# Optimization experiments

Measured on AMD Instinct MI355X. Metric: run time of the kernel, lower is better.

Reference implementation:

```python
import jax, jax.numpy as jnp
import numpy as np


def setup_inputs() -> dict:
    key = jax.random.key(0)
    ks = jax.random.split(key, 12)
    N, F, S = 50000, 256, 20          # node_num, feature_dim, samp_num
    B = 8192                          # batch of target nodes
    L1, L2 = 256, 128                 # layer1_dim, layer2_dim
    D1, D2 = 256, 256                 # dec1_dim, dec2_dim
    inv = lambda d: 1.0 / np.sqrt(d)
    return {
        "features": jax.random.normal(ks[0], (N, F), jnp.float32),
        "neigh1": jax.random.randint(ks[1], (N, S), 0, N),   # sampled neighbors (layer 1)
        "neigh2": jax.random.randint(ks[2], (B, S), 0, N),   # sampled neighbors of batch nodes
        "eps": jax.random.normal(ks[3], (B, L2), jnp.float32),
        "W1": jax.random.normal(ks[4], (L1, F), jnp.float32) * inv(F),
        "W2": jax.random.normal(ks[5], (L2, L1), jnp.float32) * inv(L1),
        "W3": jax.random.normal(ks[6], (L2, L1), jnp.float32) * inv(L1),
        "Wd1": jax.random.normal(ks[7], (D1, L2), jnp.float32) * inv(L2),
        "b1": jnp.zeros((D1,), jnp.float32),
        "Wd2": jax.random.normal(ks[8], (D2, D1), jnp.float32) * inv(D1),
        "b2": jnp.zeros((D2,), jnp.float32),
        "M1": jax.random.normal(ks[9], (D2, D2), jnp.float32) * inv(D2),
        "M2": jax.random.normal(ks[10], (D2, D2), jnp.float32) * inv(D2),
    }


def reference(features, neigh1, neigh2, eps, W1, W2, W3, Wd1, b1, Wd2, b2, M1, M2):
    # --- encode: GraphSAGE mean-aggregate, gcn=True encoder (no self-concat) ---
    # layer 1: aggregate raw features over sampled neighbors for every node
    agg1 = jnp.mean(features[neigh1], axis=1)            # [N, F]
    h1 = jax.nn.relu(agg1 @ W1.T)                        # [N, L1]
    # layer 2: aggregate layer-1 embeddings over the batch nodes' sampled neighbors
    agg2 = jnp.mean(h1[neigh2], axis=1)                  # [B, L1]
    mu = jax.nn.relu(agg2 @ W2.T)                        # [B, L2]  (enc2)
    logvar = jax.nn.relu(agg2 @ W3.T)                    # [B, L2]  (enc3)
    # --- reparameterize: std = exp(logvar), h = eps*std + mu ---
    h = eps * jnp.exp(logvar) + mu                       # [B, L2]
    # --- decode ---
    o = jnp.tanh(h @ Wd1.T + b1)                         # [B, D1]
    o = o @ Wd2.T + b2                                   # [B, D2]
    emb1 = o @ M1                                        # [B, D2]
    emb2 = o @ M2                                        # [B, D2]
    # --- inner product decoder (logits, no sigmoid) ---
    adj_without_sigmoid = emb1 @ emb2.T                  # [B, B]
    return (mu, logvar, adj_without_sigmoid)
```

## Files before the change

### kernel.cpp

```cpp
#include <hip/hip_runtime.h>
#include <cstdint>
#include <cstddef>

typedef unsigned short u16;
typedef unsigned int   u32;
typedef unsigned char  u8;
typedef __attribute__((ext_vector_type(8))) short short8;
typedef __attribute__((ext_vector_type(8))) u16   u16x8;
typedef __attribute__((ext_vector_type(4))) float f32x4;
typedef __attribute__((ext_vector_type(2))) float f32x2;
typedef __attribute__((ext_vector_type(4))) u16   u16x4;

__device__ __forceinline__ float bf2f(u16 u){
  u32 x = ((u32)u) << 16; float f; __builtin_memcpy(&f, &x, 4); return f;
}
__device__ __forceinline__ u16 f2bf(float f){
  u32 x; __builtin_memcpy(&x, &f, 4);
  x += 0x7fffu + ((x >> 16) & 1u);
  return (u16)(x >> 16);
}

__device__ __forceinline__ void gload_lds16(const u16* g, u16* l){
  __builtin_amdgcn_global_load_lds((const __attribute__((address_space(1))) void*)g,
                                   (__attribute__((address_space(3))) void*)l, 16, 0, 0);
}

__global__ __launch_bounds__(256)
void prep(const float* __restrict__ M2v, const float* __restrict__ M1v,
          const float* __restrict__ W1, const float* __restrict__ W2,
          const float* __restrict__ W3, const float* __restrict__ Wd1,
          const float* __restrict__ Wd2,
          u16* __restrict__ Gtb, u16* __restrict__ W1b, u16* __restrict__ Wcb,
          u16* __restrict__ Wd1b, u16* __restrict__ Wd2b)
{
  __shared__ u16 lds[32768];
  const int tid = threadIdx.x;
  if (blockIdx.x >= 4){
    int j = (blockIdx.x - 4) * 256 + tid;
    const float* src; u16* dst;
    if (j < 16384)                { src = W1;  dst = W1b; }
    else if ((j -= 16384) < 8192) { src = W2;  dst = Wcb; }
    else if ((j -= 8192)  < 8192) { src = W3;  dst = Wcb + 32768; }
    else if ((j -= 8192)  < 8192) { src = Wd1; dst = Wd1b; }
    else { j -= 8192; src = Wd2; dst = Wd2b; }
    float4 v = ((const float4*)src)[j];
    u16x4 o; o[0]=f2bf(v.x); o[1]=f2bf(v.y); o[2]=f2bf(v.z); o[3]=f2bf(v.w);
    ((u16x4*)dst)[j] = o;
    return;
  }
  u16* As0 = lds;         u16* As1 = lds + 8192;
  u16* Bs0 = lds + 16384; u16* Bs1 = lds + 24576;
  const int lane = tid & 63;
  const int wave = tid >> 6;
  const int wm = wave >> 1, wn = wave & 1;
  const int m0 = (blockIdx.x >> 1) << 7, n0 = (blockIdx.x & 1) << 7;

  f32x4 acc[4][4];
  #pragma unroll
  for (int a = 0; a < 4; ++a)
    #pragma unroll
    for (int b = 0; b < 4; ++b)
      acc[a][b] = (f32x4){0.f, 0.f, 0.f, 0.f};

  auto stage = [&](int buf, int kt){
    const int k0 = kt * 64;
    u16* Ad = buf ? As1 : As0;
    u16* Bd = buf ? Bs1 : Bs0;
    const int f = tid * 32;
    {
      const float* sA = M2v + (size_t)(m0 + (f >> 6)) * 256 + k0 + (f & 63);
      u16 t[32];
      #pragma unroll
      for (int q = 0; q < 8; ++q){
        float4 v = *(const float4*)(sA + q * 4);
        t[q*4]=f2bf(v.x); t[q*4+1]=f2bf(v.y); t[q*4+2]=f2bf(v.z); t[q*4+3]=f2bf(v.w);
      }
      #pragma unroll
      for (int q = 0; q < 4; ++q)
        *(u16x8*)(&Ad[f + q*8]) = *(const u16x8*)(&t[q*8]);
    }
    {
      const float* sB = M1v + (size_t)(n0 + (f >> 6)) * 256 + k0 + (f & 63);
      u16 t[32];
      #pragma unroll
      for (int q = 0; q < 8; ++q){
        float4 v = *(const float4*)(sB + q * 4);
        t[q*4]=f2bf(v.x); t[q*4+1]=f2bf(v.y); t[q*4+2]=f2bf(v.z); t[q*4+3]=f2bf(v.w);
      }
      #pragma unroll
      for (int q = 0; q < 4; ++q)
        *(u16x8*)(&Bd[f + q*8]) = *(const u16x8*)(&t[q*8]);
    }
  };

  stage(0, 0);
  __syncthreads();
  int cur = 0;
  for (int kt = 0; kt < 4; ++kt){
    if (kt < 3) stage(cur ^ 1, kt + 1);
    const u16* as = cur ? As1 : As0;
    const u16* bs = cur ? Bs1 : Bs0;
    #pragma unroll
    for (int kk = 0; kk < 2; ++kk){
      const int ko = kk * 32 + (lane >> 4) * 8;
      short8 af[4], bq[4];
      #pragma unroll
      for (int mi = 0; mi < 4; ++mi)
        af[mi] = *(const short8*)(as + (wm*64 + mi*16 + (lane & 15)) * 64 + ko);
      #pragma unroll
      for (int ni = 0; ni < 4; ++ni)
        bq[ni] = *(const short8*)(bs + (wn*64 + ni*16 + (lane & 15)) * 64 + ko);
      #pragma unroll
      for (int mi = 0; mi < 4; ++mi)
        #pragma unroll
        for (int ni = 0; ni < 4; ++ni)
          acc[mi][ni] = __builtin_amdgcn_mfma_f32_16x16x32_bf16(af[mi], bq[ni], acc[mi][ni], 0, 0, 0);
    }
    __syncthreads();
    cur ^= 1;
  }

  const int rbase = m0 + wm * 64 + ((lane >> 4) << 2);
  const int cbase = n0 + wn * 64 + (lane & 15);
  #pragma unroll
  for (int mi = 0; mi < 4; ++mi)
    #pragma unroll
    for (int ni = 0; ni < 4; ++ni){
      const int col = cbase + ni * 16;
      #pragma unroll
      for (int r = 0; r < 4; ++r)
        Gtb[(size_t)(rbase + mi * 16 + r) * 256 + col] = f2bf(acc[mi][ni][r]);
    }
}

__global__ void gather_fp8(const u32* __restrict__ rows, const int* __restrict__ idx,
                           u32* __restrict__ out, int nout){
  const int pair = blockIdx.x * 4 + (threadIdx.x >> 6);
  const int lane = threadIdx.x & 63;
  const int node0 = pair * 2;
  if (node0 >= nout) return;
  const int half = lane >> 5, l31 = lane & 31;
  const int node = node0 + half;
  const int jv = (l31 < 20) ? idx[(size_t)node * 20 + l31] : 0;
  float a[8];
  #pragma unroll
  for (int k = 0; k < 8; ++k) a[k] = 0.f;
  #pragma unroll
  for (int s = 0; s < 20; ++s){
    const int j = __shfl(jv, (lane & 32) + s, 64);
    const uint2 u = *(const uint2*)(rows + (size_t)j * 64 + l31 * 2);
    f32x2 p0 = __builtin_amdgcn_cvt_pk_f32_fp8((int)u.x, false);
    f32x2 p1 = __builtin_amdgcn_cvt_pk_f32_fp8((int)u.x, true);
    f32x2 p2 = __builtin_amdgcn_cvt_pk_f32_fp8((int)u.y, false);
    f32x2 p3 = __builtin_amdgcn_cvt_pk_f32_fp8((int)u.y, true);
    a[0]+=p0[0]; a[1]+=p0[1]; a[2]+=p1[0]; a[3]+=p1[1];
    a[4]+=p2[0]; a[5]+=p2[1]; a[6]+=p3[0]; a[7]+=p3[1];
  }
  const float inv = 0.05f;
  #pragma unroll
  for (int k = 0; k < 8; ++k) a[k] = fmaxf(a[k] * inv, 0.f);
  const int w0 = __builtin_amdgcn_cvt_pk_fp8_f32(a[0], a[1], 0, false);
  const int w1 = __builtin_amdgcn_cvt_pk_fp8_f32(a[2], a[3], 0, false);
  const int w2 = __builtin_amdgcn_cvt_pk_fp8_f32(a[4], a[5], 0, false);
  const int w3 = __builtin_amdgcn_cvt_pk_fp8_f32(a[6], a[7], 0, false);
  uint2 o;
  o.x = (w0 & 0xffffu) | ((u32)(w1 & 0xffffu) << 16);
  o.y = (w2 & 0xffffu) | ((u32)(w3 & 0xffffu) << 16);
  *(uint2*)(out + (size_t)node * 64 + l31 * 2) = o;
}

__global__ __launch_bounds__(512)
void adj_gemm(const u16* __restrict__ A, const u16* __restrict__ B,
              float* __restrict__ C)
{
  __shared__ __align__(16) u16 lds[32768];
  u16* As = lds;
  u16* Bs = lds + 16384;
  const int tid  = threadIdx.x;
  const int lane = tid & 63;
  const int wave = tid >> 6;
  const int wm = wave >> 2, wn = wave & 3;
  const int bid  = blockIdx.x;
  const int xcd  = bid & 7, slot = bid >> 3;
  const int m0 = ((xcd << 2) + (slot >> 5)) << 8;
  const int n0 = (slot & 31) << 8;

  f32x4 acc[8][4];
  #pragma unroll
  for (int a = 0; a < 8; ++a)
    #pragma unroll
    for (int b = 0; b < 4; ++b)
      acc[a][b] = (f32x4){0.f, 0.f, 0.f, 0.f};

  for (int kt = 0; kt < 4; ++kt){
    const int k0 = kt * 64;
    #pragma unroll
    for (int c = 0; c < 4; ++c){
      const int f = c * 4096 + tid * 8;
      const int row = f >> 6, ksw = (f & 63) ^ ((row & 7) << 3);
      gload_lds16(A + (size_t)(m0 + row) * 256 + k0 + ksw, As + f);
    }
    #pragma unroll
    for (int c = 0; c < 4; ++c){
      const int f = c * 4096 + tid * 8;
      const int row = f >> 6, ksw = (f & 63) ^ ((row & 7) << 3);
      gload_lds16(B + (size_t)(n0 + row) * 256 + k0 + ksw, Bs + f);
    }
    __syncthreads();
    #pragma unroll
    for (int kk = 0; kk < 2; ++kk){
      const int ko = kk * 32 + (lane >> 4) * 8;
      short8 af[8], bq[4];
      #pragma unroll
      for (int mi = 0; mi < 8; ++mi){
        const int row = wm*128 + mi*16 + (lane & 15);
        af[mi] = *(const short8*)(As + row * 64 + (ko ^ ((row & 7) << 3)));
      }
      #pragma unroll
      for (int ni = 0; ni < 4; ++ni){
        const int row = wn*64 + ni*16 + (lane & 15);
        bq[ni] = *(const short8*)(Bs + row * 64 + (ko ^ ((row & 7) << 3)));
      }
      #pragma unroll
      for (int mi = 0; mi < 8; ++mi)
        #pragma unroll
        for (int ni = 0; ni < 4; ++ni)
          acc[mi][ni] = __builtin_amdgcn_mfma_f32_16x16x32_bf16(af[mi], bq[ni], acc[mi][ni], 0, 0, 0);
    }
    __syncthreads();
  }

  float* T = (float*)lds;
  #pragma unroll
  for (int c = 0; c < 8; ++c){
    if (wm == (c >> 2)){
      #pragma unroll
      for (int mi2 = 0; mi2 < 2; ++mi2){
        const int mi = (c & 3) * 2 + mi2;
        #pragma unroll
        for (int ni = 0; ni < 4; ++ni){
          const int cl = wn*64 + ni*16 + (lane & 15);
          #pragma unroll
          for (int r = 0; r < 4; ++r){
            const int lr = mi2*16 + ((lane >> 4) << 2) + r;
            T[lr * 260 + cl] = acc[mi][ni][r];
          }
        }
      }
    }
    __syncthreads();
    #pragma unroll
    for (int q = 0; q < 4; ++q){
      const int g = q * 512 + tid;
      const int r = g >> 6, col = (g & 63) * 4;
      f32x4 v = *(const f32x4*)(T + r * 260 + col);
      __builtin_nontemporal_store(v, (f32x4*)(C + (size_t)(m0 + c*32 + r) * 8192 + n0 + col));
    }
    __syncthreads();
  }
}

__global__ __launch_bounds__(256)
void fw_gemm(const float* __restrict__ A, const u16* __restrict__ B,
             u8* __restrict__ C, int M)
{
  __shared__ u16 lds[26624];
  u16* As0 = lds;         u16* As1 = lds + 5120;
  u16* Bs0 = lds + 10240; u16* Bs1 = lds + 18432;
  const int tid  = threadIdx.x;
  const int lane = tid & 63;
  const int wave = tid >> 6;
  const int wm = wave >> 1, wn = wave & 1;
  const int m0 = blockIdx.x << 7;

  f32x4 acc[4][8];
  #pragma unroll
  for (int a = 0; a < 4; ++a)
    #pragma unroll
    for (int b = 0; b < 8; ++b)
      acc[a][b] = (f32x4){0.f, 0.f, 0.f, 0.f};

  auto stage = [&](int buf, int kt){
    const int k0 = kt * 32;
    u16* Ad = buf ? As1 : As0;
    u16* Bd = buf ? Bs1 : Bs0;
    const int f = tid * 16;
    const int row = f >> 5, ku = f & 31;
    int ra = m0 + row; if (ra >= M) ra = M - 1;
    const float* sA = A + (size_t)ra * 256 + k0 + ku;
    u16 t[16];
    #pragma unroll
    for (int q = 0; q < 4; ++q){
      float4 v = *(const float4*)(sA + q * 4);
      t[q*4]=f2bf(v.x); t[q*4+1]=f2bf(v.y); t[q*4+2]=f2bf(v.z); t[q*4+3]=f2bf(v.w);
    }
    u16* dA = Ad + row * 40 + ku;
    *(u16x8*)(dA)     = *(const u16x8*)(&t[0]);
    *(u16x8*)(dA + 8) = *(const u16x8*)(&t[8]);
    #pragma unroll
    for (int c = 0; c < 4; ++c){
      const int g = c * 2048 + tid * 8;
      const int rb = g >> 5, kb = g & 31;
      gload_lds16(B + (size_t)rb * 256 + k0 + (kb ^ ((rb & 3) << 3)),
                  Bd + c * 2048 + wave * 512);
    }
  };

  stage(0, 0);
  __syncthreads();
  int cur = 0;
  for (int kt = 0; kt < 8; ++kt){
    if (kt + 1 < 8) stage(cur ^ 1, kt + 1);
    const u16* as = cur ? As1 : As0;
    const u16* bs = cur ? Bs1 : Bs0;
    const int ko = (lane >> 4) * 8;
    short8 af[4], bq[8];
    #pragma unroll
    for (int mi = 0; mi < 4; ++mi)
      af[mi] = *(const short8*)(as + (wm*64 + mi*16 + (lane & 15)) * 40 + ko);
    #pragma unroll
    for (int ni = 0; ni < 8; ++ni){
      const int row = wn*128 + ni*16 + (lane & 15);
      bq[ni] = *(const short8*)(bs + row * 32 + (ko ^ ((row & 3) << 3)));
    }
    #pragma unroll
    for (int mi = 0; mi < 4; ++mi)
      #pragma unroll
      for (int ni = 0; ni < 8; ++ni)
        acc[mi][ni] = __builtin_amdgcn_mfma_f32_16x16x32_bf16(af[mi], bq[ni], acc[mi][ni], 0, 0, 0);
    __syncthreads();
    cur ^= 1;
  }

  const int rbase = m0 + wm * 64 + ((lane >> 4) << 2);
  const int cbase = wn * 128 + (lane & 15);
  #pragma unroll
  for (int mi = 0; mi < 4; ++mi)
    #pragma unroll
    for (int ni = 0; ni < 8; ++ni){
      const int col = cbase + ni * 16;
      #pragma unroll
      for (int r = 0; r < 4; ++r){
        const int row = rbase + mi * 16 + r;
        if (row < M){
          const float v = acc[mi][ni][r];
          const int pk = __builtin_amdgcn_cvt_pk_fp8_f32(v, v, 0, false);
          C[(size_t)row * 256 + col] = (u8)(pk & 0xff);
        }
      }
    }
}

__global__ __launch_bounds__(256)
void decoder(const u32* __restrict__ h1, const int* __restrict__ neigh2,
             const u16* __restrict__ Wcb,
             const u16* __restrict__ Wd1b, const u16* __restrict__ Wd2b,
             const u16* __restrict__ Gtb, const float* __restrict__ eps,
             const float* __restrict__ b1, const float* __restrict__ b2,
             float* __restrict__ outMu, float* __restrict__ outLv,
             u16* __restrict__ o2g, u16* __restrict__ tmpg)
{
  __shared__ u16 lds[38912];
  u16* S0 = lds;
  u16* S1 = lds + 16384;
  u16* H  = lds + 32768;
  u16* O1 = lds + 34816;
  const int tid = threadIdx.x;
  const int lane = tid & 63, wave = tid >> 6;
  const int m0 = blockIdx.x << 4;

  auto stageB = [&](const u16* G, int K, int k0, u16* dst){
    const int fb = wave * 4096 + lane * 8;
    #pragma unroll
    for (int c = 0; c < 8; ++c){
      int f = fb + c * 512;
      gload_lds16(G + (size_t)(f >> 6) * K + k0 + (f & 63), dst + wave*4096 + c*512);
    }
  };
  auto mstep16 = [&](const u16* aC, const u16* bT, f32x4 (&acc)[4]){
    #pragma unroll
    for (int kk = 0; kk < 2; ++kk){
      const int ko = kk * 32 + (lane >> 4) * 8;
      short8 af = *(const short8*)(aC + (lane & 15) * 64 + ko);
      #pragma unroll
      for (int ni = 0; ni < 4; ++ni){
        short8 bq = *(const short8*)(bT + (wave*64 + ni*16 + (lane & 15)) * 64 + ko);
        acc[ni] = __builtin_amdgcn_mfma_f32_16x16x32_bf16(af, bq, acc[ni], 0, 0, 0);
      }
    }
  };

  {
    const int half = lane >> 5, l31 = lane & 31;
    #pragma unroll
    for (int it = 0; it < 2; ++it){
      const int lrow = it * 8 + wave * 2 + half;
      const int node = m0 + lrow;
      const int jv = (l31 < 20) ? neigh2[(size_t)node * 20 + l31] : 0;
      float a[8];
      #pragma unroll
      for (int k = 0; k < 8; ++k) a[k] = 0.f;
      #pragma unroll
      for (int s = 0; s < 20; ++s){
        const int j = __shfl(jv, (lane & 32) + s, 64);
        const uint2 u = *(const uint2*)(h1 + (size_t)j * 64 + l31 * 2);
        f32x2 p0 = __builtin_amdgcn_cvt_pk_f32_fp8((int)u.x, false);
        f32x2 p1 = __builtin_amdgcn_cvt_pk_f32_fp8((int)u.x, true);
        f32x2 p2 = __builtin_amdgcn_cvt_pk_f32_fp8((int)u.y, false);
        f32x2 p3 = __builtin_amdgcn_cvt_pk_f32_fp8((int)u.y, true);
        a[0]+=p0[0]; a[1]+=p0[1]; a[2]+=p1[0]; a[3]+=p1[1];
        a[4]+=p2[0]; a[5]+=p2[1]; a[6]+=p3[0]; a[7]+=p3[1];
      }
      const float inv = 0.05f;
      u16x8 o;
      #pragma unroll
      for (int k = 0; k < 8; ++k) o[k] = f2bf(a[k] * inv);
      const int c0 = l31 * 8;
      *(u16x8*)(O1 + (c0 >> 6) * 1024 + lrow * 64 + (c0 & 63)) = o;
    }
  }

  f32x4 accm[2], accl[2];
  #pragma unroll
  for (int b = 0; b < 2; ++b){
    accm[b] = (f32x4){0.f,0.f,0.f,0.f};
    accl[b] = (f32x4){0.f,0.f,0.f,0.f};
  }
  {
    stageB(Wcb, 256, 0, S0);
    __syncthreads();
    for (int kt = 0; kt < 4; ++kt){
      if (kt < 3) stageB(Wcb, 256, (kt+1)*64, ((kt+1)&1) ? S1 : S0);
      const u16* as = O1 + kt * 1024;
      const u16* bs = (kt & 1) ? S1 : S0;
      #pragma unroll
      for (int kk = 0; kk < 2; ++kk){
        const int ko = kk * 32 + (lane >> 4) * 8;
        short8 af = *(const short8*)(as + (lane & 15) * 64 + ko);
        #pragma unroll
        for (int ni = 0; ni < 2; ++ni){
          short8 bm = *(const short8*)(bs + (wave*32 + ni*16 + (lane & 15)) * 64 + ko);
          short8 bl = *(const short8*)(bs + (128 + wave*32 + ni*16 + (lane & 15)) * 64 + ko);
          accm[ni] = __builtin_amdgcn_mfma_f32_16x16x32_bf16(af, bm, accm[ni], 0, 0, 0);
          accl[ni] = __builtin_amdgcn_mfma_f32_16x16x32_bf16(af, bl, accl[ni], 0, 0, 0);
        }
      }
      __syncthreads();
    }
  }
  {
    const int erow = (lane >> 4) << 2;
    #pragma unroll
    for (int ni = 0; ni < 2; ++ni){
      const int col = wave*32 + ni*16 + (lane & 15);
      #pragma unroll
      for (int r = 0; r < 4; ++r){
        const int lrow = erow + r;
        const size_t off = (size_t)(m0 + lrow) * 128 + col;
        const float m = fmaxf(accm[ni][r], 0.f);
        const float l = fmaxf(accl[ni][r], 0.f);
        __builtin_nontemporal_store(m, &outMu[off]);
        __builtin_nontemporal_store(l, &outLv[off]);
        H[(col >> 6) * 1024 + lrow * 64 + (col & 63)] = f2bf(eps[off] * expf(l) + m);
      }
    }
  }
  stageB(Wd1b, 128, 0, S0);
  stageB(Wd1b, 128, 64, S1);
  __syncthreads();

  const int rb = (lane >> 4) << 2;
  const int cb = wave * 64 + (lane & 15);

  {
    f32x4 acc[4];
    #pragma unroll
    for (int b = 0; b < 4; ++b) acc[b] = (f32x4){0.f,0.f,0.f,0.f};
    mstep16(H, S0, acc);
    mstep16(H + 1024, S1, acc);
    __syncthreads();
    #pragma unroll
    for (int ni = 0; ni < 4; ++ni){
      const int col = cb + ni * 16;
      const float bv = b1[col];
      #pragma unroll
      for (int r = 0; r < 4; ++r){
        const int lrow = rb + r;
        O1[(col >> 6) * 1024 + lrow * 64 + (col & 63)] = f2bf(tanhf(acc[ni][r] + bv));
      }
    }
    stageB(Wd2b, 256, 0, S0);
    __syncthreads();
  }

  {
    f32x4 acc[4];
    #pragma unroll
    for (int b = 0; b < 4; ++b) acc[b] = (f32x4){0.f,0.f,0.f,0.f};
    for (int c = 0; c < 4; ++c){
      if (c < 3) stageB(Wd2b, 256, (c+1)*64, ((c+1)&1) ? S1 : S0);
      mstep16(O1 + c*1024, (c&1) ? S1 : S0, acc);
      __syncthreads();
    }
    #pragma unroll
    for (int ni = 0; ni < 4; ++ni){
      const int col = cb + ni * 16;
      const float bv = b2[col];
      #pragma unroll
      for (int r = 0; r < 4; ++r){
        const int lrow = rb + r;
        O1[(col >> 6) * 1024 + lrow * 64 + (col & 63)] = f2bf(acc[ni][r] + bv);
      }
    }
    __syncthreads();
    stageB(Gtb, 256, 0, S0);
    #pragma unroll
    for (int q = 0; q < 2; ++q){
      const int e = q * 2048 + tid * 8;
      const int lrow = e >> 8, col = e & 255;
      *(u16x8*)(o2g + (size_t)(m0 + lrow) * 256 + col) =
        *(const u16x8*)(O1 + (col >> 6) * 1024 + lrow * 64 + (col & 63));
    }
    __syncthreads();
  }

  {
    f32x4 acc[4];
    #pragma unroll
    for (int b = 0; b < 4; ++b) acc[b] = (f32x4){0.f,0.f,0.f,0.f};
    for (int c = 0; c < 4; ++c){
      if (c < 3) stageB(Gtb, 256, (c+1)*64, ((c+1)&1) ? S1 : S0);
      mstep16(O1 + c*1024, (c&1) ? S1 : S0, acc);
      __syncthreads();
    }
    #pragma unroll
    for (int ni = 0; ni < 4; ++ni){
      const int col = cb + ni * 16;
      #pragma unroll
      for (int r = 0; r < 4; ++r){
        const int lrow = rb + r;
        tmpg[(size_t)(m0 + lrow) * 256 + col] = f2bf(acc[ni][r]);
      }
    }
  }
}

extern "C" void kernel_launch(void* const* d_in, const int* in_sizes, int n_in,
                              void* d_out, int out_size, void* d_ws, size_t ws_size,
                              hipStream_t stream){
  const float* features = (const float*)d_in[0];
  const int*   neigh1   = (const int*)  d_in[1];
  const int*   neigh2   = (const int*)  d_in[2];
  const float* eps      = (const float*)d_in[3];
  const float* W1       = (const float*)d_in[4];
  const float* W2       = (const float*)d_in[5];
  const float* W3       = (const float*)d_in[6];
  const float* Wd1      = (const float*)d_in[7];
  const float* b1       = (const float*)d_in[8];
  const float* Wd2      = (const float*)d_in[9];
  const float* b2       = (const float*)d_in[10];
  const float* M1       = (const float*)d_in[11];
  const float* M2       = (const float*)d_in[12];
  float* out = (float*)d_out;
  char*  ws  = (char*)d_ws;

  u8*  FW8  = (u8*)(ws);
  u32* h18  = (u32*)(ws + 25600000);
  u16* o2g  = (u16*)(ws + 14680064);
  u16* tmpg = (u16*)(ws + 18874368);
  u16* W1b  = (u16*)(ws + 51200000);
  u16* Wcb  = W1b  + 65536;
  u16* Wd1b = Wcb  + 65536;
  u16* Wd2b = Wd1b + 32768;
  u16* Gtb  = Wd2b + 65536;

  prep<<<228, 256, 0, stream>>>(M2, M1, W1, W2, W3, Wd1, Wd2,
                                Gtb, W1b, Wcb, Wd1b, Wd2b);
  fw_gemm<<<391, 256, 0, stream>>>(features, W1b, FW8, 50000);
  gather_fp8<<<6250, 256, 0, stream>>>((const u32*)FW8, neigh1, h18, 50000);
  decoder<<<512, 256, 0, stream>>>(h18, neigh2, Wcb, Wd1b, Wd2b, Gtb, eps, b1, b2,
                                   out, out + 1048576, o2g, tmpg);
  adj_gemm<<<1024, 512, 0, stream>>>(tmpg, o2g, out + 2097152);
}
```

Baseline: 158.8 us.

## Merge weight prep into features GEMM kernel and single-buffer decoder LDS

Folds the separate prep kernel into the features×W1 GEMM kernel as extra blocks. The W1 fp32→bf16 conversion now happens inside each GEMM block's staging instead of via a pre-converted buffer, and the M2·M1ᵀ product runs as four extra blocks without double buffering. This removes one kernel launch and the dependency between the two kernels, but each of the 391 GEMM blocks now re-reads and converts fp32 W1 in registers instead of using async LDS loads. The decoder drops its double-buffered weight staging in favour of a single buffer with an extra barrier per step. That shrinks LDS use and may raise occupancy, at the cost of losing load/compute overlap.

```diff
diff --git a/kernel.cpp b/kernel.cpp
--- a/kernel.cpp
+++ b/kernel.cpp
@@ -26,110 +26,192 @@
 }
 
 __global__ __launch_bounds__(256)
-void prep(const float* __restrict__ M2v, const float* __restrict__ M1v,
-          const float* __restrict__ W1, const float* __restrict__ W2,
-          const float* __restrict__ W3, const float* __restrict__ Wd1,
-          const float* __restrict__ Wd2,
-          u16* __restrict__ Gtb, u16* __restrict__ W1b, u16* __restrict__ Wcb,
-          u16* __restrict__ Wd1b, u16* __restrict__ Wd2b)
+void fwprep(const float* __restrict__ F, const float* __restrict__ W1f,
+            const float* __restrict__ M2v, const float* __restrict__ M1v,
+            const float* __restrict__ W2, const float* __restrict__ W3,
+            const float* __restrict__ Wd1, const float* __restrict__ Wd2,
+            u8* __restrict__ FW8, u16* __restrict__ Gtb, u16* __restrict__ Wcb,
+            u16* __restrict__ Wd1b, u16* __restrict__ Wd2b, int M)
 {
-  __shared__ u16 lds[32768];
-  const int tid = threadIdx.x;
-  if (blockIdx.x >= 4){
-    int j = (blockIdx.x - 4) * 256 + tid;
+  __shared__ u16 lds[26624];
+  const int tid  = threadIdx.x;
+  const int bid  = blockIdx.x;
+
+  if (bid >= 395){
+    int j = (bid - 395) * 256 + tid;
     const float* src; u16* dst;
-    if (j < 16384)                { src = W1;  dst = W1b; }
-    else if ((j -= 16384) < 8192) { src = W2;  dst = Wcb; }
-    else if ((j -= 8192)  < 8192) { src = W3;  dst = Wcb + 32768; }
-    else if ((j -= 8192)  < 8192) { src = Wd1; dst = Wd1b; }
+    if (j < 8192)                 { src = W2;  dst = Wcb; }
+    else if ((j -= 8192) < 8192)  { src = W3;  dst = Wcb + 32768; }
+    else if ((j -= 8192) < 8192)  { src = Wd1; dst = Wd1b; }
     else { j -= 8192; src = Wd2; dst = Wd2b; }
     float4 v = ((const float4*)src)[j];
     u16x4 o; o[0]=f2bf(v.x); o[1]=f2bf(v.y); o[2]=f2bf(v.z); o[3]=f2bf(v.w);
     ((u16x4*)dst)[j] = o;
     return;
   }
-  u16* As0 = lds;         u16* As1 = lds + 8192;
-  u16* Bs0 = lds + 16384; u16* Bs1 = lds + 24576;
+
   const int lane = tid & 63;
   const int wave = tid >> 6;
+
+  if (bid >= 391){
+    u16* As = lds;
+    u16* Bs = lds + 8192;
+    const int g = bid - 391;
+    const int wm = wave >> 1, wn = wave & 1;
+    const int m0 = (g >> 1) << 7, n0 = (g & 1) << 7;
+
+    f32x4 acc[4][4];
+    #pragma unroll
+    for (int a = 0; a < 4; ++a)
+      #pragma unroll
+      for (int b = 0; b < 4; ++b)
+        acc[a][b] = (f32x4){0.f, 0.f, 0.f, 0.f};
+
+    for (int kt = 0; kt < 4; ++kt){
+      const int k0 = kt * 64;
+      const int f = tid * 32;
+      {
+        const float* sA = M2v + (size_t)(m0 + (f >> 6)) * 256 + k0 + (f & 63);
+        u16 t[32];
+        #pragma unroll
+        for (int q = 0; q < 8; ++q){
+          float4 v = *(const float4*)(sA + q * 4);
+          t[q*4]=f2bf(v.x); t[q*4+1]=f2bf(v.y); t[q*4+2]=f2bf(v.z); t[q*4+3]=f2bf(v.w);
+        }
+        #pragma unroll
+        for (int q = 0; q < 4; ++q)
+          *(u16x8*)(&As[f + q*8]) = *(const u16x8*)(&t[q*8]);
+      }
+      {
+        const float* sB = M1v + (size_t)(n0 + (f >> 6)) * 256 + k0 + (f & 63);
+        u16 t[32];
+        #pragma unroll
+        for (int q = 0; q < 8; ++q){
+          float4 v = *(const float4*)(sB + q * 4);
+          t[q*4]=f2bf(v.x); t[q*4+1]=f2bf(v.y); t[q*4+2]=f2bf(v.z); t[q*4+3]=f2bf(v.w);
+        }
+        #pragma unroll
+        for (int q = 0; q < 4; ++q)
+          *(u16x8*)(&Bs[f + q*8]) = *(const u16x8*)(&t[q*8]);
+      }
+      __syncthreads();
+      #pragma unroll
+      for (int kk = 0; kk < 2; ++kk){
+        const int ko = kk * 32 + (lane >> 4) * 8;
+        short8 af[4], bq[4];
+        #pragma unroll
+        for (int mi = 0; mi < 4; ++mi)
+          af[mi] = *(const short8*)(As + (wm*64 + mi*16 + (lane & 15)) * 64 + ko);
+        #pragma unroll
+        for (int ni = 0; ni < 4; ++ni)
+          bq[ni] = *(const short8*)(Bs + (wn*64 + ni*16 + (lane & 15)) * 64 + ko);
+        #pragma unroll
+        for (int mi = 0; mi < 4; ++mi)
+          #pragma unroll
+          for (int ni = 0; ni < 4; ++ni)
+            acc[mi][ni] = __builtin_amdgcn_mfma_f32_16x16x32_bf16(af[mi], bq[ni], acc[mi][ni], 0, 0, 0);
+      }
+      __syncthreads();
+    }
+
+    const int rbase = m0 + wm * 64 + ((lane >> 4) << 2);
+    const int cbase = n0 + wn * 64 + (lane & 15);
+    #pragma unroll
+    for (int mi = 0; mi < 4; ++mi)
+      #pragma unroll
+      for (int ni = 0; ni < 4; ++ni){
+        const int col = cbase + ni * 16;
+        #pragma unroll
+        for (int r = 0; r < 4; ++r)
+          Gtb[(size_t)(rbase + mi * 16 + r) * 256 + col] = f2bf(acc[mi][ni][r]);
+      }
+    return;
+  }
+
+  u16* As0 = lds;         u16* As1 = lds + 5120;
+  u16* Bs0 = lds + 10240; u16* Bs1 = lds + 18432;
   const int wm = wave >> 1, wn = wave & 1;
-  const int m0 = (blockIdx.x >> 1) << 7, n0 = (blockIdx.x & 1) << 7;
-
-  f32x4 acc[4][4];
+  const int m0 = bid << 7;
+
+  f32x4 acc[4][8];
   #pragma unroll
   for (int a = 0; a < 4; ++a)
     #pragma unroll
-    for (int b = 0; b < 4; ++b)
+    for (int b = 0; b < 8; ++b)
       acc[a][b] = (f32x4){0.f, 0.f, 0.f, 0.f};
 
   auto stage = [&](int buf, int kt){
-    const int k0 = kt * 64;
+    const int k0 = kt * 32;
     u16* Ad = buf ? As1 : As0;
     u16* Bd = buf ? Bs1 : Bs0;
-    const int f = tid * 32;
-    {
-      const float* sA = M2v + (size_t)(m0 + (f >> 6)) * 256 + k0 + (f & 63);
-      u16 t[32];
-      #pragma unroll
-      for (int q = 0; q < 8; ++q){
-        float4 v = *(const float4*)(sA + q * 4);
-        t[q*4]=f2bf(v.x); t[q*4+1]=f2bf(v.y); t[q*4+2]=f2bf(v.z); t[q*4+3]=f2bf(v.w);
-      }
-      #pragma unroll
-      for (int q = 0; q < 4; ++q)
-        *(u16x8*)(&Ad[f + q*8]) = *(const u16x8*)(&t[q*8]);
-    }
-    {
-      const float* sB = M1v + (size_t)(n0 + (f >> 6)) * 256 + k0 + (f & 63);
-      u16 t[32];
-      #pragma unroll
-      for (int q = 0; q < 8; ++q){
-        float4 v = *(const float4*)(sB + q * 4);
-        t[q*4]=f2bf(v.x); t[q*4+1]=f2bf(v.y); t[q*4+2]=f2bf(v.z); t[q*4+3]=f2bf(v.w);
-      }
-      #pragma unroll
-      for (int q = 0; q < 4; ++q)
-        *(u16x8*)(&Bd[f + q*8]) = *(const u16x8*)(&t[q*8]);
-    }
+    const int f = tid * 16;
+    const int row = f >> 5, ku = f & 31;
+    int ra = m0 + row; if (ra >= M) ra = M - 1;
+    const float* sA = F + (size_t)ra * 256 + k0 + ku;
+    u16 t[16];
+    #pragma unroll
+    for (int q = 0; q < 4; ++q){
+      float4 v = *(const float4*)(sA + q * 4);
+      t[q*4]=f2bf(v.x); t[q*4+1]=f2bf(v.y); t[q*4+2]=f2bf(v.z); t[q*4+3]=f2bf(v.w);
+    }
+    u16* dA = Ad + row * 40 + ku;
+    *(u16x8*)(dA)     = *(const u16x8*)(&t[0]);
+    *(u16x8*)(dA + 8) = *(const u16x8*)(&t[8]);
+    const float* sB = W1f + (size_t)tid * 256 + k0;
+    u16 tb[32];
+    #pragma unroll
+    for (int q = 0; q < 8; ++q){
+      float4 v = *(const float4*)(sB + q * 4);
+      tb[q*4]=f2bf(v.x); tb[q*4+1]=f2bf(v.y); tb[q*4+2]=f2bf(v.z); tb[q*4+3]=f2bf(v.w);
+    }
+    const int sw = (tid & 3) << 3;
+    #pragma unroll
+    for (int q = 0; q < 4; ++q)
+      *(u16x8*)(&Bd[tid * 32 + ((q * 8) ^ sw)]) = *(const u16x8*)(&tb[q*8]);
   };
 
   stage(0, 0);
   __syncthreads();
   int cur = 0;
-  for (int kt = 0; kt < 4; ++kt){
-    if (kt < 3) stage(cur ^ 1, kt + 1);
+  for (int kt = 0; kt < 8; ++kt){
+    if (kt + 1 < 8) stage(cur ^ 1, kt + 1);
     const u16* as = cur ? As1 : As0;
     const u16* bs = cur ? Bs1 : Bs0;
-    #pragma unroll
-    for (int kk = 0; kk < 2; ++kk){
-      const int ko = kk * 32 + (lane >> 4) * 8;
-      short8 af[4], bq[4];
-      #pragma unroll
-      for (int mi = 0; mi < 4; ++mi)
-        af[mi] = *(const short8*)(as + (wm*64 + mi*16 + (lane & 15)) * 64 + ko);
-      #pragma unroll
-      for (int ni = 0; ni < 4; ++ni)
-        bq[ni] = *(const short8*)(bs + (wn*64 + ni*16 + (lane & 15)) * 64 + ko);
-      #pragma unroll
-      for (int mi = 0; mi < 4; ++mi)
-        #pragma unroll
-        for (int ni = 0; ni < 4; ++ni)
-          acc[mi][ni] = __builtin_amdgcn_mfma_f32_16x16x32_bf16(af[mi], bq[ni], acc[mi][ni], 0, 0, 0);
-    }
+    const int ko = (lane >> 4) * 8;
+    short8 af[4], bq[8];
+    #pragma unroll
+    for (int mi = 0; mi < 4; ++mi)
+      af[mi] = *(const short8*)(as + (wm*64 + mi*16 + (lane & 15)) * 40 + ko);
+    #pragma unroll
+    for (int ni = 0; ni < 8; ++ni){
+      const int row = wn*128 + ni*16 + (lane & 15);
+      bq[ni] = *(const short8*)(bs + row * 32 + (ko ^ ((row & 3) << 3)));
+    }
+    #pragma unroll
+    for (int mi = 0; mi < 4; ++mi)
+      #pragma unroll
+      for (int ni = 0; ni < 8; ++ni)
+        acc[mi][ni] = __builtin_amdgcn_mfma_f32_16x16x32_bf16(af[mi], bq[ni], acc[mi][ni], 0, 0, 0);
     __syncthreads();
     cur ^= 1;
   }
 
   const int rbase = m0 + wm * 64 + ((lane >> 4) << 2);
-  const int cbase = n0 + wn * 64 + (lane & 15);
+  const int cbase = wn * 128 + (lane & 15);
   #pragma unroll
   for (int mi = 0; mi < 4; ++mi)
     #pragma unroll
-    for (int ni = 0; ni < 4; ++ni){
+    for (int ni = 0; ni < 8; ++ni){
       const int col = cbase + ni * 16;
       #pragma unroll
-      for (int r = 0; r < 4; ++r)
-        Gtb[(size_t)(rbase + mi * 16 + r) * 256 + col] = f2bf(acc[mi][ni][r]);
+      for (int r = 0; r < 4; ++r){
+        const int row = rbase + mi * 16 + r;
+        if (row < M){
+          const float v = acc[mi][ni][r];
+          const int pk = __builtin_amdgcn_cvt_pk_fp8_f32(v, v, 0, false);
+          FW8[(size_t)row * 256 + col] = (u8)(pk & 0xff);
+        }
+      }
     }
 }
 
@@ -261,97 +343,6 @@
 }
 
 __global__ __launch_bounds__(256)
-void fw_gemm(const float* __restrict__ A, const u16* __restrict__ B,
-             u8* __restrict__ C, int M)
-{
-  __shared__ u16 lds[26624];
-  u16* As0 = lds;         u16* As1 = lds + 5120;
-  u16* Bs0 = lds + 10240; u16* Bs1 = lds + 18432;
-  const int tid  = threadIdx.x;
-  const int lane = tid & 63;
-  const int wave = tid >> 6;
-  const int wm = wave >> 1, wn = wave & 1;
-  const int m0 = blockIdx.x << 7;
-
-  f32x4 acc[4][8];
-  #pragma unroll
-  for (int a = 0; a < 4; ++a)
-    #pragma unroll
-    for (int b = 0; b < 8; ++b)
-      acc[a][b] = (f32x4){0.f, 0.f, 0.f, 0.f};
-
-  auto stage = [&](int buf, int kt){
-    const int k0 = kt * 32;
-    u16* Ad = buf ? As1 : As0;
-    u16* Bd = buf ? Bs1 : Bs0;
-    const int f = tid * 16;
-    const int row = f >> 5, ku = f & 31;
-    int ra = m0 + row; if (ra >= M) ra = M - 1;
-    const float* sA = A + (size_t)ra * 256 + k0 + ku;
-    u16 t[16];
-    #pragma unroll
-    for (int q = 0; q < 4; ++q){
-      float4 v = *(const float4*)(sA + q * 4);
-      t[q*4]=f2bf(v.x); t[q*4+1]=f2bf(v.y); t[q*4+2]=f2bf(v.z); t[q*4+3]=f2bf(v.w);
-    }
-    u16* dA = Ad + row * 40 + ku;
-    *(u16x8*)(dA)     = *(const u16x8*)(&t[0]);
-    *(u16x8*)(dA + 8) = *(const u16x8*)(&t[8]);
-    #pragma unroll
-    for (int c = 0; c < 4; ++c){
-      const int g = c * 2048 + tid * 8;
-      const int rb = g >> 5, kb = g & 31;
-      gload_lds16(B + (size_t)rb * 256 + k0 + (kb ^ ((rb & 3) << 3)),
-                  Bd + c * 2048 + wave * 512);
-    }
-  };
-
-  stage(0, 0);
-  __syncthreads();
-  int cur = 0;
-  for (int kt = 0; kt < 8; ++kt){
-    if (kt + 1 < 8) stage(cur ^ 1, kt + 1);
-    const u16* as = cur ? As1 : As0;
-    const u16* bs = cur ? Bs1 : Bs0;
-    const int ko = (lane >> 4) * 8;
-    short8 af[4], bq[8];
-    #pragma unroll
-    for (int mi = 0; mi < 4; ++mi)
-      af[mi] = *(const short8*)(as + (wm*64 + mi*16 + (lane & 15)) * 40 + ko);
-    #pragma unroll
-    for (int ni = 0; ni < 8; ++ni){
-      const int row = wn*128 + ni*16 + (lane & 15);
-      bq[ni] = *(const short8*)(bs + row * 32 + (ko ^ ((row & 3) << 3)));
-    }
-    #pragma unroll
-    for (int mi = 0; mi < 4; ++mi)
-      #pragma unroll
-      for (int ni = 0; ni < 8; ++ni)
-        acc[mi][ni] = __builtin_amdgcn_mfma_f32_16x16x32_bf16(af[mi], bq[ni], acc[mi][ni], 0, 0, 0);
-    __syncthreads();
-    cur ^= 1;
-  }
-
-  const int rbase = m0 + wm * 64 + ((lane >> 4) << 2);
-  const int cbase = wn * 128 + (lane & 15);
-  #pragma unroll
-  for (int mi = 0; mi < 4; ++mi)
-    #pragma unroll
-    for (int ni = 0; ni < 8; ++ni){
-      const int col = cbase + ni * 16;
-      #pragma unroll
-      for (int r = 0; r < 4; ++r){
-        const int row = rbase + mi * 16 + r;
-        if (row < M){
-          const float v = acc[mi][ni][r];
-          const int pk = __builtin_amdgcn_cvt_pk_fp8_f32(v, v, 0, false);
-          C[(size_t)row * 256 + col] = (u8)(pk & 0xff);
-        }
-      }
-    }
-}
-
-__global__ __launch_bounds__(256)
 void decoder(const u32* __restrict__ h1, const int* __restrict__ neigh2,
              const u16* __restrict__ Wcb,
              const u16* __restrict__ Wd1b, const u16* __restrict__ Wd2b,
@@ -360,31 +351,30 @@
              float* __restrict__ outMu, float* __restrict__ outLv,
              u16* __restrict__ o2g, u16* __restrict__ tmpg)
 {
-  __shared__ u16 lds[38912];
-  u16* S0 = lds;
-  u16* S1 = lds + 16384;
-  u16* H  = lds + 32768;
-  u16* O1 = lds + 34816;
+  __shared__ u16 lds[22528];
+  u16* S  = lds;
+  u16* H  = lds + 16384;
+  u16* O1 = lds + 18432;
   const int tid = threadIdx.x;
   const int lane = tid & 63, wave = tid >> 6;
   const int m0 = blockIdx.x << 4;
 
-  auto stageB = [&](const u16* G, int K, int k0, u16* dst){
+  auto stageB = [&](const u16* G, int K, int k0){
     const int fb = wave * 4096 + lane * 8;
     #pragma unroll
     for (int c = 0; c < 8; ++c){
       int f = fb + c * 512;
-      gload_lds16(G + (size_t)(f >> 6) * K + k0 + (f & 63), dst + wave*4096 + c*512);
+      gload_lds16(G + (size_t)(f >> 6) * K + k0 + (f & 63), S + wave*4096 + c*512);
     }
   };
-  auto mstep16 = [&](const u16* aC, const u16* bT, f32x4 (&acc)[4]){
+  auto mstep16 = [&](const u16* aC, f32x4 (&acc)[4]){
     #pragma unroll
     for (int kk = 0; kk < 2; ++kk){
       const int ko = kk * 32 + (lane >> 4) * 8;
       short8 af = *(const short8*)(aC + (lane & 15) * 64 + ko);
       #pragma unroll
       for (int ni = 0; ni < 4; ++ni){
-        short8 bq = *(const short8*)(bT + (wave*64 + ni*16 + (lane & 15)) * 64 + ko);
+        short8 bq = *(const short8*)(S + (wave*64 + ni*16 + (lane & 15)) * 64 + ko);
         acc[ni] = __builtin_amdgcn_mfma_f32_16x16x32_bf16(af, bq, acc[ni], 0, 0, 0);
       }
     }
@@ -426,27 +416,23 @@
     accm[b] = (f32x4){0.f,0.f,0.f,0.f};
     accl[b] = (f32x4){0.f,0.f,0.f,0.f};
   }
-  {
-    stageB(Wcb, 256, 0, S0);
-    __syncthreads();
-    for (int kt = 0; kt < 4; ++kt){
-      if (kt < 3) stageB(Wcb, 256, (kt+1)*64, ((kt+1)&1) ? S1 : S0);
-      const u16* as = O1 + kt * 1024;
-      const u16* bs = (kt & 1) ? S1 : S0;
-      #pragma unroll
-      for (int kk = 0; kk < 2; ++kk){
-        const int ko = kk * 32 + (lane >> 4) * 8;
-        short8 af = *(const short8*)(as + (lane & 15) * 64 + ko);
-        #pragma unroll
-        for (int ni = 0; ni < 2; ++ni){
-          short8 bm = *(const short8*)(bs + (wave*32 + ni*16 + (lane & 15)) * 64 + ko);
-          short8 bl = *(const short8*)(bs + (128 + wave*32 + ni*16 + (lane & 15)) * 64 + ko);
-          accm[ni] = __builtin_amdgcn_mfma_f32_16x16x32_bf16(af, bm, accm[ni], 0, 0, 0);
-          accl[ni] = __builtin_amdgcn_mfma_f32_16x16x32_bf16(af, bl, accl[ni], 0, 0, 0);
-        }
-      }
-      __syncthreads();
-    }
+  for (int kt = 0; kt < 4; ++kt){
+    stageB(Wcb, 256, kt * 64);
+    __syncthreads();
+    const u16* as = O1 + kt * 1024;
+    #pragma unroll
+    for (int kk = 0; kk < 2; ++kk){
+      const int ko = kk * 32 + (lane >> 4) * 8;
+      short8 af = *(const short8*)(as + (lane & 15) * 64 + ko);
+      #pragma unroll
+      for (int ni = 0; ni < 2; ++ni){
+        short8 bm = *(const short8*)(S + (wave*32 + ni*16 + (lane & 15)) * 64 + ko);
+        short8 bl = *(const short8*)(S + (128 + wave*32 + ni*16 + (lane & 15)) * 64 + ko);
+        accm[ni] = __builtin_amdgcn_mfma_f32_16x16x32_bf16(af, bm, accm[ni], 0, 0, 0);
+        accl[ni] = __builtin_amdgcn_mfma_f32_16x16x32_bf16(af, bl, accl[ni], 0, 0, 0);
+      }
+    }
+    __syncthreads();
   }
   {
     const int erow = (lane >> 4) << 2;
@@ -465,9 +451,6 @@
       }
     }
   }
-  stageB(Wd1b, 128, 0, S0);
-  stageB(Wd1b, 128, 64, S1);
-  __syncthreads();
 
   const int rb = (lane >> 4) << 2;
   const int cb = wave * 64 + (lane & 15);
@@ -476,20 +459,21 @@
     f32x4 acc[4];
     #pragma unroll
     for (int b = 0; b < 4; ++b) acc[b] = (f32x4){0.f,0.f,0.f,0.f};
-    mstep16(H, S0, acc);
-    mstep16(H + 1024, S1, acc);
-    __syncthreads();
+    #pragma unroll
+    for (int c = 0; c < 2; ++c){
+      stageB(Wd1b, 128, c * 64);
+      __syncthreads();
+      mstep16(H + c * 1024, acc);
+      __syncthreads();
+    }
     #pragma unroll
     for (int ni = 0; ni < 4; ++ni){
       const int col = cb + ni * 16;
       const float bv = b1[col];
       #pragma unroll
-      for (int r = 0; r < 4; ++r){
-        const int lrow = rb + r;
-        O1[(col >> 6) * 1024 + lrow * 64 + (col & 63)] = f2bf(tanhf(acc[ni][r] + bv));
-      }
-    }
-    stageB(Wd2b, 256, 0, S0);
+      for (int r = 0; r < 4; ++r)
+        O1[(col >> 6) * 1024 + (rb + r) * 64 + (col & 63)] = f2bf(tanhf(acc[ni][r] + bv));
+    }
     __syncthreads();
   }
 
@@ -498,8 +482,9 @@
     #pragma unroll
     for (int b = 0; b < 4; ++b) acc[b] = (f32x4){0.f,0.f,0.f,0.f};
     for (int c = 0; c < 4; ++c){
-      if (c < 3) stageB(Wd2b, 256, (c+1)*64, ((c+1)&1) ? S1 : S0);
-      mstep16(O1 + c*1024, (c&1) ? S1 : S0, acc);
+      stageB(Wd2b, 256, c * 64);
+      __syncthreads();
+      mstep16(O1 + c * 1024, acc);
       __syncthreads();
     }
     #pragma unroll
@@ -507,13 +492,10 @@
       const int col = cb + ni * 16;
       const float bv = b2[col];
       #pragma unroll
-      for (int r = 0; r < 4; ++r){
-        const int lrow = rb + r;
-        O1[(col >> 6) * 1024 + lrow * 64 + (col & 63)] = f2bf(acc[ni][r] + bv);
-      }
-    }
-    __syncthreads();
-    stageB(Gtb, 256, 0, S0);
+      for (int r = 0; r < 4; ++r)
+        O1[(col >> 6) * 1024 + (rb + r) * 64 + (col & 63)] = f2bf(acc[ni][r] + bv);
+    }
+    __syncthreads();
     #pragma unroll
     for (int q = 0; q < 2; ++q){
       const int e = q * 2048 + tid * 8;
@@ -521,7 +503,6 @@
       *(u16x8*)(o2g + (size_t)(m0 + lrow) * 256 + col) =
         *(const u16x8*)(O1 + (col >> 6) * 1024 + lrow * 64 + (col & 63));
     }
-    __syncthreads();
   }
 
   {
@@ -529,18 +510,17 @@
     #pragma unroll
     for (int b = 0; b < 4; ++b) acc[b] = (f32x4){0.f,0.f,0.f,0.f};
     for (int c = 0; c < 4; ++c){
-      if (c < 3) stageB(Gtb, 256, (c+1)*64, ((c+1)&1) ? S1 : S0);
-      mstep16(O1 + c*1024, (c&1) ? S1 : S0, acc);
+      stageB(Gtb, 256, c * 64);
+      __syncthreads();
+      mstep16(O1 + c * 1024, acc);
       __syncthreads();
     }
     #pragma unroll
     for (int ni = 0; ni < 4; ++ni){
       const int col = cb + ni * 16;
       #pragma unroll
-      for (int r = 0; r < 4; ++r){
-        const int lrow = rb + r;
-        tmpg[(size_t)(m0 + lrow) * 256 + col] = f2bf(acc[ni][r]);
-      }
+      for (int r = 0; r < 4; ++r)
+        tmpg[(size_t)(m0 + rb + r) * 256 + col] = f2bf(acc[ni][r]);
     }
   }
 }
@@ -574,9 +554,8 @@
   u16* Wd2b = Wd1b + 32768;
   u16* Gtb  = Wd2b + 65536;
 
-  prep<<<228, 256, 0, stream>>>(M2, M1, W1, W2, W3, Wd1, Wd2,
-                                Gtb, W1b, Wcb, Wd1b, Wd2b);
-  fw_gemm<<<391, 256, 0, stream>>>(features, W1b, FW8, 50000);
+  fwprep<<<555, 256, 0, stream>>>(features, W1, M2, M1, W2, W3, Wd1, Wd2,
+                                  FW8, Gtb, Wcb, Wd1b, Wd2b, 50000);
   gather_fp8<<<6250, 256, 0, stream>>>((const u32*)FW8, neigh1, h18, 50000);
   decoder<<<512, 256, 0, stream>>>(h18, neigh2, Wcb, Wd1b, Wd2b, Gtb, eps, b1, b2,
                                    out, out + 1048576, o2g, tmpg);
```

After: 171.9 us. 1.08x slower.
